# Kernel optimization log

Hardware: AMD Instinct MI355X
Metric: run time of the kernel (lower is better)

Reference implementation:

```python
import jax, jax.numpy as jnp
import numpy as np

D_MODEL = 1024
D_HEAD = 128


def setup_inputs() -> dict:
    key = jax.random.key(0)
    kx, kq, kk, kv, ko = jax.random.split(key, 5)
    x = jax.random.normal(kx, (4, 2048, D_MODEL), dtype=jnp.float32)
    # xavier-uniform-ish init scale
    s_in = (6.0 / (D_MODEL + D_HEAD)) ** 0.5
    wq = jax.random.uniform(kq, (D_MODEL, D_HEAD), minval=-s_in, maxval=s_in, dtype=jnp.float32)
    wk = jax.random.uniform(kk, (D_MODEL, D_HEAD), minval=-s_in, maxval=s_in, dtype=jnp.float32)
    wv = jax.random.uniform(kv, (D_MODEL, D_HEAD), minval=-s_in, maxval=s_in, dtype=jnp.float32)
    wo = jax.random.uniform(ko, (D_HEAD, D_MODEL), minval=-s_in, maxval=s_in, dtype=jnp.float32)
    return {"x": x, "wq": wq, "wk": wk, "wv": wv, "wo": wo}


def reference(x, wq, wk, wv, wo):
    # x: [b, s, d_model]
    s = x.shape[1]
    scale = 1.0 / (D_HEAD ** 0.5)
    q = jnp.einsum('bsd,dh->bsh', x, wq)
    k = jnp.einsum('bsd,dh->bsh', x, wk)
    v = jnp.einsum('bsd,dh->bsh', x, wv)
    scores = jnp.einsum('bqh,bkh->bqk', q, k) * scale  # [b, s, s]
    causal = jnp.tril(jnp.ones((s, s), dtype=bool))
    scores = jnp.where(causal, scores, -jnp.inf)
    attn = jax.nn.softmax(scores, axis=-1)
    ctx = jnp.einsum('bqk,bkh->bqh', attn, v)
    return jnp.einsum('bsh,hd->bsd', ctx, wo)
```

## Files before the change

kernel.cpp:

```cpp
#include <hip/hip_runtime.h>
#include <hip/hip_bf16.h>

typedef _Float16 half8 __attribute__((ext_vector_type(8)));
typedef _Float16 half4_t __attribute__((ext_vector_type(4)));
typedef _Float16 half2_t __attribute__((ext_vector_type(2)));
typedef float floatx4 __attribute__((ext_vector_type(4)));

#define MFMA16(a, b, c) __builtin_amdgcn_mfma_f32_16x16x32_f16(a, b, c, 0, 0, 0)
#define MASKVAL (-30000.0f)

#define QSCALE 0.1275261529f

__global__ __launch_bounds__(256) void transpose_convert(
    const float* __restrict__ wq, const float* __restrict__ wk,
    const float* __restrict__ wv, const float* __restrict__ wo,
    _Float16* __restrict__ wqt, _Float16* __restrict__ wkt,
    _Float16* __restrict__ wvt, _Float16* __restrict__ wot) {
  __shared__ float T[32][36];
  int bx = blockIdx.x, tid = threadIdx.x;
  const float* src;
  _Float16* dst;
  int R, C, r0, c0;
  if (bx < 384) {
    int p = bx >> 7, t = bx & 127;
    src = (p == 0) ? wq : (p == 1) ? wk : wv;
    dst = (p == 0) ? wqt : (p == 1) ? wkt : wvt;
    R = 1024; C = 128;
    r0 = (t & 31) * 32; c0 = (t >> 5) * 32;
  } else {
    int t = bx - 384;
    src = wo; dst = wot;
    R = 128; C = 1024;
    r0 = (t & 3) * 32; c0 = (t >> 2) * 32;
  }
  {
    int row = tid >> 3, c4 = (tid & 7) * 4;
    float4 f = *(const float4*)&src[(size_t)(r0 + row) * C + c0 + c4];
    T[row][c4] = f.x; T[row][c4 + 1] = f.y; T[row][c4 + 2] = f.z; T[row][c4 + 3] = f.w;
  }
  __syncthreads();
  {
    int cc = tid >> 3, r4 = (tid & 7) * 4;
    half4_t h;
    h[0] = (_Float16)T[r4 + 0][cc];
    h[1] = (_Float16)T[r4 + 1][cc];
    h[2] = (_Float16)T[r4 + 2][cc];
    h[3] = (_Float16)T[r4 + 3][cc];
    *(half4_t*)&dst[(size_t)(c0 + cc) * R + r0 + r4] = h;
  }
}

__global__ __launch_bounds__(256) void qkv_gemm(
    const float* __restrict__ x, const _Float16* __restrict__ wqt,
    const _Float16* __restrict__ wkt, const _Float16* __restrict__ wvt,
    _Float16* __restrict__ Qh, _Float16* __restrict__ Kh,
    _Float16* __restrict__ Vt) {
  __shared__ _Float16 A_lds[64 * 72];
  __shared__ _Float16 B_lds[128 * 72];
  int tid = threadIdx.x;
  int w = tid >> 6, lane = tid & 63, quad = lane >> 4, l16 = lane & 15;
  int m0 = blockIdx.x * 64;
  int proj = blockIdx.y;
  const _Float16* wt = (proj == 0) ? wqt : (proj == 1) ? wkt : wvt;
  floatx4 zero = {0.f, 0.f, 0.f, 0.f};
  floatx4 acc[8];
#pragma unroll
  for (int t = 0; t < 8; t++) acc[t] = zero;

  int arow = tid >> 2, akk = (tid & 3) * 16;
  int bn = tid >> 1, bkk = (tid & 1) * 32;

  for (int k0 = 0; k0 < 1024; k0 += 64) {
    {
      const float* s = x + (size_t)(m0 + arow) * 1024 + k0 + akk;
      float4 f0 = *(const float4*)(s);
      float4 f1 = *(const float4*)(s + 4);
      float4 f2 = *(const float4*)(s + 8);
      float4 f3 = *(const float4*)(s + 12);
      half8 h0, h1;
      h0[0] = (_Float16)f0.x; h0[1] = (_Float16)f0.y; h0[2] = (_Float16)f0.z; h0[3] = (_Float16)f0.w;
      h0[4] = (_Float16)f1.x; h0[5] = (_Float16)f1.y; h0[6] = (_Float16)f1.z; h0[7] = (_Float16)f1.w;
      h1[0] = (_Float16)f2.x; h1[1] = (_Float16)f2.y; h1[2] = (_Float16)f2.z; h1[3] = (_Float16)f2.w;
      h1[4] = (_Float16)f3.x; h1[5] = (_Float16)f3.y; h1[6] = (_Float16)f3.z; h1[7] = (_Float16)f3.w;
      *(half8*)&A_lds[arow * 72 + akk] = h0;
      *(half8*)&A_lds[arow * 72 + akk + 8] = h1;
    }
#pragma unroll
    for (int i = 0; i < 4; i++)
      *(half8*)&B_lds[bn * 72 + bkk + i * 8] =
          *(const half8*)&wt[(size_t)bn * 1024 + k0 + bkk + i * 8];
    __syncthreads();
    half8 a[2];
#pragma unroll
    for (int c = 0; c < 2; c++) a[c] = *(const half8*)&A_lds[(w * 16 + l16) * 72 + c * 32 + quad * 8];
#pragma unroll
    for (int t = 0; t < 8; t++)
#pragma unroll
      for (int c = 0; c < 2; c++) {
        half8 b = *(const half8*)&B_lds[(t * 16 + l16) * 72 + c * 32 + quad * 8];
        acc[t] = MFMA16(a[c], b, acc[t]);
      }
    __syncthreads();
  }
#pragma unroll
  for (int t = 0; t < 8; t++)
#pragma unroll
    for (int r = 0; r < 4; r++) {
      int row = m0 + w * 16 + quad * 4 + r;
      int col = t * 16 + l16;
      float v = acc[t][r];
      if (proj == 0)
        Qh[(size_t)row * 128 + col] = (_Float16)(v * QSCALE);
      else if (proj == 1)
        Kh[(size_t)row * 128 + col] = (_Float16)v;
      else {
        int bb = row >> 11, s = row & 2047;
        Vt[((size_t)(bb * 128 + col)) * 2048 + s] = (_Float16)v;
      }
    }
}

__global__ __launch_bounds__(256) void attn_partial(
    const _Float16* __restrict__ Qh, const _Float16* __restrict__ Kh,
    const _Float16* __restrict__ Vt, _Float16* __restrict__ Opart,
    float* __restrict__ Ml) {
  __shared__ _Float16 K_lds[64 * 136];
  __shared__ _Float16 V_lds[128 * 72];
  __shared__ _Float16 P_lds[4 * 16 * 76];
  int tid = threadIdx.x;
  int w = tid >> 6, lane = tid & 63, quad = lane >> 4, l16 = lane & 15;
  int kc = blockIdx.x;
  int qt = 31 - (int)blockIdx.y;
  int b = blockIdx.z;
  int q0 = qt * 64;
  int nkc = (q0 + 319) >> 8;
  if (kc >= nkc) return;
  int sidx = (b * 32 + qt) * 8 + kc;
  int ks0 = kc * 256;
  int kend = ks0 + 256 < q0 + 64 ? ks0 + 256 : q0 + 64;
  int qw0 = q0 + w * 16;

  const _Float16* Kb = Kh + (size_t)b * 2048 * 128;
  const _Float16* Vb = Vt + (size_t)b * 128 * 2048;

  half8 aq[4];
  {
    const _Float16* qbase = Qh + (size_t)(b * 2048 + qw0 + l16) * 128;
#pragma unroll
    for (int c = 0; c < 4; c++) aq[c] = *(const half8*)&qbase[c * 32 + quad * 8];
  }

  float m_r[4], l_r[4];
  floatx4 zero = {0.f, 0.f, 0.f, 0.f};
  floatx4 O[8];
#pragma unroll
  for (int r = 0; r < 4; r++) { m_r[r] = MASKVAL; l_r[r] = 0.f; }
#pragma unroll
  for (int t = 0; t < 8; t++) O[t] = zero;

  int krow = tid >> 2, kof = (tid & 3) * 32;
  int vh = tid & 127, vof = (tid >> 7) * 32;

  for (int ks = ks0; ks < kend; ks += 64) {
#pragma unroll
    for (int i = 0; i < 4; i++)
      *(half8*)&K_lds[krow * 136 + kof + i * 8] =
          *(const half8*)&Kb[(size_t)(ks + krow) * 128 + kof + i * 8];
#pragma unroll
    for (int i = 0; i < 4; i++)
      *(half8*)&V_lds[vh * 72 + vof + i * 8] =
          *(const half8*)&Vb[(size_t)vh * 2048 + ks + vof + i * 8];
    __syncthreads();

    if (ks <= qw0) {
      floatx4 sa[4];
#pragma unroll
      for (int t = 0; t < 4; t++) sa[t] = zero;
#pragma unroll
      for (int t = 0; t < 4; t++)
#pragma unroll
        for (int c = 0; c < 4; c++) {
          half8 bk = *(const half8*)&K_lds[(t * 16 + l16) * 136 + c * 32 + quad * 8];
          sa[t] = MFMA16(aq[c], bk, sa[t]);
        }

      bool domask = (ks + 63 > qw0);
      float p[4][4];
#pragma unroll
      for (int r = 0; r < 4; r++) {
        int query = qw0 + quad * 4 + r;
        float mx = m_r[r];
#pragma unroll
        for (int t = 0; t < 4; t++) {
          float s = sa[t][r];
          if (domask && (ks + t * 16 + l16 > query)) s = MASKVAL;
          p[t][r] = s;
          mx = fmaxf(mx, s);
        }
#pragma unroll
        for (int off = 1; off < 16; off <<= 1) mx = fmaxf(mx, __shfl_xor(mx, off));
        float alpha = exp2f(m_r[r] - mx);
        float rs = 0.f;
#pragma unroll
        for (int t = 0; t < 4; t++) {
          float e = exp2f(p[t][r] - mx);
          p[t][r] = e;
          rs += e;
        }
#pragma unroll
        for (int off = 1; off < 16; off <<= 1) rs += __shfl_xor(rs, off);
        l_r[r] = alpha * l_r[r] + rs;
        m_r[r] = mx;
#pragma unroll
        for (int t = 0; t < 8; t++) O[t][r] *= alpha;
      }

#pragma unroll
      for (int r = 0; r < 4; r++)
#pragma unroll
        for (int t = 0; t < 4; t++)
          P_lds[w * 16 * 76 + (quad * 4 + r) * 76 + t * 16 + l16] = (_Float16)p[t][r];

#pragma unroll
      for (int c2 = 0; c2 < 2; c2++) {
        half8 ap = *(const half8*)&P_lds[w * 16 * 76 + l16 * 76 + c2 * 32 + quad * 8];
#pragma unroll
        for (int t = 0; t < 8; t++) {
          half8 bv = *(const half8*)&V_lds[(t * 16 + l16) * 72 + c2 * 32 + quad * 8];
          O[t] = MFMA16(ap, bv, O[t]);
        }
      }
    }
    __syncthreads();
  }

  size_t obase = (size_t)sidx * 8192;
#pragma unroll
  for (int t = 0; t < 8; t++)
#pragma unroll
    for (int r = 0; r < 4; r++)
      Opart[obase + (size_t)(w * 16 + quad * 4 + r) * 128 + t * 16 + l16] = (_Float16)O[t][r];
  if (l16 == 0)
#pragma unroll
    for (int r = 0; r < 4; r++) {
      int row = w * 16 + quad * 4 + r;
      Ml[(size_t)sidx * 128 + row * 2] = m_r[r];
      Ml[(size_t)sidx * 128 + row * 2 + 1] = l_r[r];
    }
}

__global__ __launch_bounds__(256) void attn_combine(
    const _Float16* __restrict__ Opart, const float* __restrict__ Ml,
    _Float16* __restrict__ ctx) {
  int tid = threadIdx.x;
  int w = tid >> 6, lane = tid & 63;
  int row = blockIdx.x * 4 + w;
  int b = row >> 11, s = row & 2047;
  int qt = s >> 6, ri = s & 63;
  int nkc = (qt * 64 + 319) >> 8;
  int sidx0 = (b * 32 + qt) * 8;
  float m[8], l[8];
  float M = MASKVAL;
  for (int i = 0; i < nkc; i++) {
    m[i] = Ml[(size_t)(sidx0 + i) * 128 + ri * 2];
    l[i] = Ml[(size_t)(sidx0 + i) * 128 + ri * 2 + 1];
    M = fmaxf(M, m[i]);
  }
  float L = 0.f, sc[8];
  for (int i = 0; i < nkc; i++) {
    sc[i] = exp2f(m[i] - M);
    L += l[i] * sc[i];
  }
  float inv = 1.f / L;
  float a0 = 0.f, a1 = 0.f;
  for (int i = 0; i < nkc; i++) {
    half2_t o = *(const half2_t*)&Opart[(size_t)(sidx0 + i) * 8192 + (size_t)ri * 128 + lane * 2];
    a0 += sc[i] * (float)o[0];
    a1 += sc[i] * (float)o[1];
  }
  half2_t hv;
  hv[0] = (_Float16)(a0 * inv);
  hv[1] = (_Float16)(a1 * inv);
  *(half2_t*)&ctx[(size_t)row * 128 + lane * 2] = hv;
}

__global__ __launch_bounds__(256) void out_gemm(
    const _Float16* __restrict__ ctx, const _Float16* __restrict__ wot,
    float* __restrict__ out) {
  __shared__ _Float16 A_lds[64 * 136];
  __shared__ _Float16 B_lds[128 * 136];
  int tid = threadIdx.x;
  int w = tid >> 6, lane = tid & 63, quad = lane >> 4, l16 = lane & 15;
  int m0 = blockIdx.x * 64, n0 = blockIdx.y * 128;
  {
    int row = tid >> 2, kk = (tid & 3) * 32;
#pragma unroll
    for (int i = 0; i < 4; i++)
      *(half8*)&A_lds[row * 136 + kk + i * 8] =
          *(const half8*)&ctx[(size_t)(m0 + row) * 128 + kk + i * 8];
  }
  {
    int n = tid >> 1, kk = (tid & 1) * 64;
#pragma unroll
    for (int i = 0; i < 8; i++)
      *(half8*)&B_lds[n * 136 + kk + i * 8] =
          *(const half8*)&wot[(size_t)(n0 + n) * 128 + kk + i * 8];
  }
  __syncthreads();
  floatx4 zero = {0.f, 0.f, 0.f, 0.f};
  floatx4 acc[8];
#pragma unroll
  for (int t = 0; t < 8; t++) acc[t] = zero;
  half8 a[4];
#pragma unroll
  for (int c = 0; c < 4; c++) a[c] = *(const half8*)&A_lds[(w * 16 + l16) * 136 + c * 32 + quad * 8];
#pragma unroll
  for (int t = 0; t < 8; t++)
#pragma unroll
    for (int c = 0; c < 4; c++) {
      half8 b = *(const half8*)&B_lds[(t * 16 + l16) * 136 + c * 32 + quad * 8];
      acc[t] = MFMA16(a[c], b, acc[t]);
    }
#pragma unroll
  for (int t = 0; t < 8; t++)
#pragma unroll
    for (int r = 0; r < 4; r++) {
      int row = m0 + w * 16 + quad * 4 + r;
      out[(size_t)row * 1024 + n0 + t * 16 + l16] = acc[t][r];
    }
}

extern "C" void kernel_launch(void* const* d_in, const int* in_sizes, int n_in,
                              void* d_out, int out_size, void* d_ws, size_t ws_size,
                              hipStream_t stream) {
  const float* x = (const float*)d_in[0];
  const float* wq = (const float*)d_in[1];
  const float* wk = (const float*)d_in[2];
  const float* wv = (const float*)d_in[3];
  const float* wo = (const float*)d_in[4];
  char* ws = (char*)d_ws;
  _Float16* wqt = (_Float16*)(ws + 0);
  _Float16* wkt = (_Float16*)(ws + 262144);
  _Float16* wvt = (_Float16*)(ws + 524288);
  _Float16* wot = (_Float16*)(ws + 786432);
  _Float16* Qh  = (_Float16*)(ws + 1048576);
  _Float16* Kh  = (_Float16*)(ws + 1048576 + 2097152);
  _Float16* Vt  = (_Float16*)(ws + 1048576 + 2 * 2097152);
  _Float16* ctxh = (_Float16*)(ws + 1048576 + 3 * 2097152);
  _Float16* Opart = (_Float16*)(ws + 9437184);
  float* Ml = (float*)(ws + 9437184 + 16777216);
  float* out = (float*)d_out;

  transpose_convert<<<512, 256, 0, stream>>>(wq, wk, wv, wo, wqt, wkt, wvt, wot);
  qkv_gemm<<<dim3(128, 3), 256, 0, stream>>>(x, wqt, wkt, wvt, Qh, Kh, Vt);
  attn_partial<<<dim3(8, 32, 4), 256, 0, stream>>>(Qh, Kh, Vt, Opart, Ml);
  attn_combine<<<2048, 256, 0, stream>>>(Opart, Ml, ctxh);
  out_gemm<<<dim3(128, 8), 256, 0, stream>>>(ctxh, wot, out);
}
```

Baseline: 171.6 us.

## Pre-convert x to fp16, widen GEMM K-tile, split attention into single 128-key chunks

Adds a prep pass that converts x to fp16 and folds the Q scale into the transposed Wq weights, so the QKV GEMM loads fp16 directly with a 128-wide K tile. Attention partials now use one 128-key chunk per block (16 splits instead of 8), with no inner loop or online rescaling, and skip fully-masked tiles. Combine is simplified to a single pass. This raises parallelism and cuts per-block serial work, at the cost of an extra write and read of x in fp16 and more partial outputs for the combine step to read.

```diff
diff --git a/kernel.cpp b/kernel.cpp
--- a/kernel.cpp
+++ b/kernel.cpp
@@ -8,27 +8,40 @@
 
 #define MFMA16(a, b, c) __builtin_amdgcn_mfma_f32_16x16x32_f16(a, b, c, 0, 0, 0)
 #define MASKVAL (-30000.0f)
-
 #define QSCALE 0.1275261529f
 
-__global__ __launch_bounds__(256) void transpose_convert(
-    const float* __restrict__ wq, const float* __restrict__ wk,
-    const float* __restrict__ wv, const float* __restrict__ wo,
+__global__ __launch_bounds__(256) void prep(
+    const float* __restrict__ x, const float* __restrict__ wq,
+    const float* __restrict__ wk, const float* __restrict__ wv,
+    const float* __restrict__ wo, _Float16* __restrict__ xh,
     _Float16* __restrict__ wqt, _Float16* __restrict__ wkt,
     _Float16* __restrict__ wvt, _Float16* __restrict__ wot) {
+  int bx = blockIdx.x, tid = threadIdx.x;
+  if (bx < 4096) {
+    size_t idx = (size_t)bx * 2048 + tid * 8;
+    float4 f0 = *(const float4*)&x[idx];
+    float4 f1 = *(const float4*)&x[idx + 4];
+    half8 h;
+    h[0] = (_Float16)f0.x; h[1] = (_Float16)f0.y; h[2] = (_Float16)f0.z; h[3] = (_Float16)f0.w;
+    h[4] = (_Float16)f1.x; h[5] = (_Float16)f1.y; h[6] = (_Float16)f1.z; h[7] = (_Float16)f1.w;
+    *(half8*)&xh[idx] = h;
+    return;
+  }
   __shared__ float T[32][36];
-  int bx = blockIdx.x, tid = threadIdx.x;
   const float* src;
   _Float16* dst;
   int R, C, r0, c0;
-  if (bx < 384) {
-    int p = bx >> 7, t = bx & 127;
+  float sc = 1.0f;
+  if (bx < 4480) {
+    int b2 = bx - 4096;
+    int p = b2 >> 7, t = b2 & 127;
     src = (p == 0) ? wq : (p == 1) ? wk : wv;
     dst = (p == 0) ? wqt : (p == 1) ? wkt : wvt;
+    if (p == 0) sc = QSCALE;
     R = 1024; C = 128;
     r0 = (t & 31) * 32; c0 = (t >> 5) * 32;
   } else {
-    int t = bx - 384;
+    int t = bx - 4480;
     src = wo; dst = wot;
     R = 128; C = 1024;
     r0 = (t & 3) * 32; c0 = (t >> 2) * 32;
@@ -42,21 +55,21 @@
   {
     int cc = tid >> 3, r4 = (tid & 7) * 4;
     half4_t h;
-    h[0] = (_Float16)T[r4 + 0][cc];
-    h[1] = (_Float16)T[r4 + 1][cc];
-    h[2] = (_Float16)T[r4 + 2][cc];
-    h[3] = (_Float16)T[r4 + 3][cc];
+    h[0] = (_Float16)(T[r4 + 0][cc] * sc);
+    h[1] = (_Float16)(T[r4 + 1][cc] * sc);
+    h[2] = (_Float16)(T[r4 + 2][cc] * sc);
+    h[3] = (_Float16)(T[r4 + 3][cc] * sc);
     *(half4_t*)&dst[(size_t)(c0 + cc) * R + r0 + r4] = h;
   }
 }
 
 __global__ __launch_bounds__(256) void qkv_gemm(
-    const float* __restrict__ x, const _Float16* __restrict__ wqt,
+    const _Float16* __restrict__ xh, const _Float16* __restrict__ wqt,
     const _Float16* __restrict__ wkt, const _Float16* __restrict__ wvt,
     _Float16* __restrict__ Qh, _Float16* __restrict__ Kh,
     _Float16* __restrict__ Vt) {
-  __shared__ _Float16 A_lds[64 * 72];
-  __shared__ _Float16 B_lds[128 * 72];
+  __shared__ _Float16 A_lds[64 * 136];
+  __shared__ _Float16 B_lds[128 * 136];
   int tid = threadIdx.x;
   int w = tid >> 6, lane = tid & 63, quad = lane >> 4, l16 = lane & 15;
   int m0 = blockIdx.x * 64;
@@ -67,37 +80,28 @@
 #pragma unroll
   for (int t = 0; t < 8; t++) acc[t] = zero;
 
-  int arow = tid >> 2, akk = (tid & 3) * 16;
-  int bn = tid >> 1, bkk = (tid & 1) * 32;
-
-  for (int k0 = 0; k0 < 1024; k0 += 64) {
-    {
-      const float* s = x + (size_t)(m0 + arow) * 1024 + k0 + akk;
-      float4 f0 = *(const float4*)(s);
-      float4 f1 = *(const float4*)(s + 4);
-      float4 f2 = *(const float4*)(s + 8);
-      float4 f3 = *(const float4*)(s + 12);
-      half8 h0, h1;
-      h0[0] = (_Float16)f0.x; h0[1] = (_Float16)f0.y; h0[2] = (_Float16)f0.z; h0[3] = (_Float16)f0.w;
-      h0[4] = (_Float16)f1.x; h0[5] = (_Float16)f1.y; h0[6] = (_Float16)f1.z; h0[7] = (_Float16)f1.w;
-      h1[0] = (_Float16)f2.x; h1[1] = (_Float16)f2.y; h1[2] = (_Float16)f2.z; h1[3] = (_Float16)f2.w;
-      h1[4] = (_Float16)f3.x; h1[5] = (_Float16)f3.y; h1[6] = (_Float16)f3.z; h1[7] = (_Float16)f3.w;
-      *(half8*)&A_lds[arow * 72 + akk] = h0;
-      *(half8*)&A_lds[arow * 72 + akk + 8] = h1;
-    }
+  int arow = tid >> 2, akk = (tid & 3) * 32;
+  int brow = tid >> 1, bkk = (tid & 1) * 64;
+
+  for (int k0 = 0; k0 < 1024; k0 += 128) {
 #pragma unroll
     for (int i = 0; i < 4; i++)
-      *(half8*)&B_lds[bn * 72 + bkk + i * 8] =
-          *(const half8*)&wt[(size_t)bn * 1024 + k0 + bkk + i * 8];
+      *(half8*)&A_lds[arow * 136 + akk + i * 8] =
+          *(const half8*)&xh[(size_t)(m0 + arow) * 1024 + k0 + akk + i * 8];
+#pragma unroll
+    for (int i = 0; i < 8; i++)
+      *(half8*)&B_lds[brow * 136 + bkk + i * 8] =
+          *(const half8*)&wt[(size_t)brow * 1024 + k0 + bkk + i * 8];
     __syncthreads();
-    half8 a[2];
-#pragma unroll
-    for (int c = 0; c < 2; c++) a[c] = *(const half8*)&A_lds[(w * 16 + l16) * 72 + c * 32 + quad * 8];
+    half8 a[4];
+#pragma unroll
+    for (int c = 0; c < 4; c++)
+      a[c] = *(const half8*)&A_lds[(w * 16 + l16) * 136 + c * 32 + quad * 8];
 #pragma unroll
     for (int t = 0; t < 8; t++)
 #pragma unroll
-      for (int c = 0; c < 2; c++) {
-        half8 b = *(const half8*)&B_lds[(t * 16 + l16) * 72 + c * 32 + quad * 8];
+      for (int c = 0; c < 4; c++) {
+        half8 b = *(const half8*)&B_lds[(t * 16 + l16) * 136 + c * 32 + quad * 8];
         acc[t] = MFMA16(a[c], b, acc[t]);
       }
     __syncthreads();
@@ -108,14 +112,14 @@
     for (int r = 0; r < 4; r++) {
       int row = m0 + w * 16 + quad * 4 + r;
       int col = t * 16 + l16;
-      float v = acc[t][r];
+      _Float16 v = (_Float16)acc[t][r];
       if (proj == 0)
-        Qh[(size_t)row * 128 + col] = (_Float16)(v * QSCALE);
+        Qh[(size_t)row * 128 + col] = v;
       else if (proj == 1)
-        Kh[(size_t)row * 128 + col] = (_Float16)v;
+        Kh[(size_t)row * 128 + col] = v;
       else {
         int bb = row >> 11, s = row & 2047;
-        Vt[((size_t)(bb * 128 + col)) * 2048 + s] = (_Float16)v;
+        Vt[((size_t)(bb * 128 + col)) * 2048 + s] = v;
       }
     }
 }
@@ -124,115 +128,116 @@
     const _Float16* __restrict__ Qh, const _Float16* __restrict__ Kh,
     const _Float16* __restrict__ Vt, _Float16* __restrict__ Opart,
     float* __restrict__ Ml) {
-  __shared__ _Float16 K_lds[64 * 136];
-  __shared__ _Float16 V_lds[128 * 72];
-  __shared__ _Float16 P_lds[4 * 16 * 76];
+  __shared__ _Float16 K_lds[128 * 136];
+  __shared__ _Float16 V_lds[128 * 136];
   int tid = threadIdx.x;
   int w = tid >> 6, lane = tid & 63, quad = lane >> 4, l16 = lane & 15;
   int kc = blockIdx.x;
   int qt = 31 - (int)blockIdx.y;
   int b = blockIdx.z;
+  int nkc = (qt + 2) >> 1;
+  if (kc >= nkc) return;
   int q0 = qt * 64;
-  int nkc = (q0 + 319) >> 8;
-  if (kc >= nkc) return;
-  int sidx = (b * 32 + qt) * 8 + kc;
-  int ks0 = kc * 256;
-  int kend = ks0 + 256 < q0 + 64 ? ks0 + 256 : q0 + 64;
+  int k0 = kc * 128;
   int qw0 = q0 + w * 16;
+  int sidx = (b * 32 + qt) * 16 + kc;
+  bool domask = (kc == nkc - 1);
 
   const _Float16* Kb = Kh + (size_t)b * 2048 * 128;
   const _Float16* Vb = Vt + (size_t)b * 128 * 2048;
 
+  {
+    int row = tid >> 1, koff = (tid & 1) * 64;
+#pragma unroll
+    for (int i = 0; i < 8; i++)
+      *(half8*)&K_lds[row * 136 + koff + i * 8] =
+          *(const half8*)&Kb[(size_t)(k0 + row) * 128 + koff + i * 8];
+#pragma unroll
+    for (int i = 0; i < 8; i++)
+      *(half8*)&V_lds[row * 136 + koff + i * 8] =
+          *(const half8*)&Vb[(size_t)row * 2048 + k0 + koff + i * 8];
+  }
+
   half8 aq[4];
   {
     const _Float16* qbase = Qh + (size_t)(b * 2048 + qw0 + l16) * 128;
 #pragma unroll
     for (int c = 0; c < 4; c++) aq[c] = *(const half8*)&qbase[c * 32 + quad * 8];
   }
+  __syncthreads();
+
+  int ntl = ((qw0 + 15 - k0) >> 4) + 1;
+  ntl = ntl > 8 ? 8 : ntl;
+
+  floatx4 zero = {0.f, 0.f, 0.f, 0.f};
+  floatx4 sa[8];
+#pragma unroll
+  for (int t = 0; t < 8; t++) sa[t] = zero;
+#pragma unroll
+  for (int t = 0; t < 8; t++)
+    if (t < ntl) {
+#pragma unroll
+      for (int c = 0; c < 4; c++) {
+        half8 bk = *(const half8*)&K_lds[(t * 16 + l16) * 136 + c * 32 + quad * 8];
+        sa[t] = MFMA16(aq[c], bk, sa[t]);
+      }
+    }
 
   float m_r[4], l_r[4];
-  floatx4 zero = {0.f, 0.f, 0.f, 0.f};
+  float p[8][4];
+#pragma unroll
+  for (int r = 0; r < 4; r++) {
+    int query = qw0 + quad * 4 + r;
+    float mx = MASKVAL;
+#pragma unroll
+    for (int t = 0; t < 8; t++) {
+      if (t < ntl) {
+        float s = sa[t][r];
+        if (domask && (k0 + t * 16 + l16 > query)) s = MASKVAL;
+        p[t][r] = s;
+        mx = fmaxf(mx, s);
+      } else {
+        p[t][r] = 0.f;
+      }
+    }
+#pragma unroll
+    for (int off = 1; off < 16; off <<= 1) mx = fmaxf(mx, __shfl_xor(mx, off));
+    float rs = 0.f;
+#pragma unroll
+    for (int t = 0; t < 8; t++)
+      if (t < ntl) {
+        float e = exp2f(p[t][r] - mx);
+        p[t][r] = e;
+        rs += e;
+      }
+#pragma unroll
+    for (int off = 1; off < 16; off <<= 1) rs += __shfl_xor(rs, off);
+    m_r[r] = mx;
+    l_r[r] = rs;
+  }
+
+  __syncthreads();
+  _Float16* P = K_lds + w * 16 * 136;
+#pragma unroll
+  for (int r = 0; r < 4; r++)
+#pragma unroll
+    for (int t = 0; t < 8; t++)
+      P[(quad * 4 + r) * 136 + t * 16 + l16] = (_Float16)p[t][r];
+
   floatx4 O[8];
 #pragma unroll
-  for (int r = 0; r < 4; r++) { m_r[r] = MASKVAL; l_r[r] = 0.f; }
-#pragma unroll
   for (int t = 0; t < 8; t++) O[t] = zero;
-
-  int krow = tid >> 2, kof = (tid & 3) * 32;
-  int vh = tid & 127, vof = (tid >> 7) * 32;
-
-  for (int ks = ks0; ks < kend; ks += 64) {
-#pragma unroll
-    for (int i = 0; i < 4; i++)
-      *(half8*)&K_lds[krow * 136 + kof + i * 8] =
-          *(const half8*)&Kb[(size_t)(ks + krow) * 128 + kof + i * 8];
-#pragma unroll
-    for (int i = 0; i < 4; i++)
-      *(half8*)&V_lds[vh * 72 + vof + i * 8] =
-          *(const half8*)&Vb[(size_t)vh * 2048 + ks + vof + i * 8];
-    __syncthreads();
-
-    if (ks <= qw0) {
-      floatx4 sa[4];
-#pragma unroll
-      for (int t = 0; t < 4; t++) sa[t] = zero;
-#pragma unroll
-      for (int t = 0; t < 4; t++)
-#pragma unroll
-        for (int c = 0; c < 4; c++) {
-          half8 bk = *(const half8*)&K_lds[(t * 16 + l16) * 136 + c * 32 + quad * 8];
-          sa[t] = MFMA16(aq[c], bk, sa[t]);
-        }
-
-      bool domask = (ks + 63 > qw0);
-      float p[4][4];
-#pragma unroll
-      for (int r = 0; r < 4; r++) {
-        int query = qw0 + quad * 4 + r;
-        float mx = m_r[r];
-#pragma unroll
-        for (int t = 0; t < 4; t++) {
-          float s = sa[t][r];
-          if (domask && (ks + t * 16 + l16 > query)) s = MASKVAL;
-          p[t][r] = s;
-          mx = fmaxf(mx, s);
-        }
-#pragma unroll
-        for (int off = 1; off < 16; off <<= 1) mx = fmaxf(mx, __shfl_xor(mx, off));
-        float alpha = exp2f(m_r[r] - mx);
-        float rs = 0.f;
-#pragma unroll
-        for (int t = 0; t < 4; t++) {
-          float e = exp2f(p[t][r] - mx);
-          p[t][r] = e;
-          rs += e;
-        }
-#pragma unroll
-        for (int off = 1; off < 16; off <<= 1) rs += __shfl_xor(rs, off);
-        l_r[r] = alpha * l_r[r] + rs;
-        m_r[r] = mx;
-#pragma unroll
-        for (int t = 0; t < 8; t++) O[t][r] *= alpha;
-      }
-
-#pragma unroll
-      for (int r = 0; r < 4; r++)
-#pragma unroll
-        for (int t = 0; t < 4; t++)
-          P_lds[w * 16 * 76 + (quad * 4 + r) * 76 + t * 16 + l16] = (_Float16)p[t][r];
-
-#pragma unroll
-      for (int c2 = 0; c2 < 2; c2++) {
-        half8 ap = *(const half8*)&P_lds[w * 16 * 76 + l16 * 76 + c2 * 32 + quad * 8];
-#pragma unroll
-        for (int t = 0; t < 8; t++) {
-          half8 bv = *(const half8*)&V_lds[(t * 16 + l16) * 72 + c2 * 32 + quad * 8];
-          O[t] = MFMA16(ap, bv, O[t]);
-        }
-      }
-    }
-    __syncthreads();
-  }
+  int nc2 = (ntl + 1) >> 1;
+#pragma unroll
+  for (int c2 = 0; c2 < 4; c2++)
+    if (c2 < nc2) {
+      half8 ap = *(const half8*)&P[l16 * 136 + c2 * 32 + quad * 8];
+#pragma unroll
+      for (int t = 0; t < 8; t++) {
+        half8 bv = *(const half8*)&V_lds[(t * 16 + l16) * 136 + c2 * 32 + quad * 8];
+        O[t] = MFMA16(ap, bv, O[t]);
+      }
+    }
 
   size_t obase = (size_t)sidx * 8192;
 #pragma unroll
@@ -257,27 +262,22 @@
   int row = blockIdx.x * 4 + w;
   int b = row >> 11, s = row & 2047;
   int qt = s >> 6, ri = s & 63;
-  int nkc = (qt * 64 + 319) >> 8;
-  int sidx0 = (b * 32 + qt) * 8;
-  float m[8], l[8];
+  int nkc = (qt + 2) >> 1;
+  int sidx0 = (b * 32 + qt) * 16;
   float M = MASKVAL;
+  for (int i = 0; i < nkc; i++)
+    M = fmaxf(M, Ml[(size_t)(sidx0 + i) * 128 + ri * 2]);
+  float L = 0.f, a0 = 0.f, a1 = 0.f;
   for (int i = 0; i < nkc; i++) {
-    m[i] = Ml[(size_t)(sidx0 + i) * 128 + ri * 2];
-    l[i] = Ml[(size_t)(sidx0 + i) * 128 + ri * 2 + 1];
-    M = fmaxf(M, m[i]);
-  }
-  float L = 0.f, sc[8];
-  for (int i = 0; i < nkc; i++) {
-    sc[i] = exp2f(m[i] - M);
-    L += l[i] * sc[i];
+    float mi = Ml[(size_t)(sidx0 + i) * 128 + ri * 2];
+    float li = Ml[(size_t)(sidx0 + i) * 128 + ri * 2 + 1];
+    float sc = exp2f(mi - M);
+    L += li * sc;
+    half2_t o = *(const half2_t*)&Opart[(size_t)(sidx0 + i) * 8192 + (size_t)ri * 128 + lane * 2];
+    a0 += sc * (float)o[0];
+    a1 += sc * (float)o[1];
   }
   float inv = 1.f / L;
-  float a0 = 0.f, a1 = 0.f;
-  for (int i = 0; i < nkc; i++) {
-    half2_t o = *(const half2_t*)&Opart[(size_t)(sidx0 + i) * 8192 + (size_t)ri * 128 + lane * 2];
-    a0 += sc[i] * (float)o[0];
-    a1 += sc[i] * (float)o[1];
-  }
   half2_t hv;
   hv[0] = (_Float16)(a0 * inv);
   hv[1] = (_Float16)(a1 * inv);
@@ -343,17 +343,18 @@
   _Float16* wkt = (_Float16*)(ws + 262144);
   _Float16* wvt = (_Float16*)(ws + 524288);
   _Float16* wot = (_Float16*)(ws + 786432);
-  _Float16* Qh  = (_Float16*)(ws + 1048576);
-  _Float16* Kh  = (_Float16*)(ws + 1048576 + 2097152);
-  _Float16* Vt  = (_Float16*)(ws + 1048576 + 2 * 2097152);
-  _Float16* ctxh = (_Float16*)(ws + 1048576 + 3 * 2097152);
-  _Float16* Opart = (_Float16*)(ws + 9437184);
-  float* Ml = (float*)(ws + 9437184 + 16777216);
+  _Float16* xh  = (_Float16*)(ws + 1048576);
+  _Float16* Qh  = (_Float16*)(ws + 17825792);
+  _Float16* Kh  = (_Float16*)(ws + 19922944);
+  _Float16* Vt  = (_Float16*)(ws + 22020096);
+  _Float16* ctxh = (_Float16*)(ws + 24117248);
+  _Float16* Opart = (_Float16*)(ws + 26214400);
+  float* Ml = (float*)(ws + 59768832);
   float* out = (float*)d_out;
 
-  transpose_convert<<<512, 256, 0, stream>>>(wq, wk, wv, wo, wqt, wkt, wvt, wot);
-  qkv_gemm<<<dim3(128, 3), 256, 0, stream>>>(x, wqt, wkt, wvt, Qh, Kh, Vt);
-  attn_partial<<<dim3(8, 32, 4), 256, 0, stream>>>(Qh, Kh, Vt, Opart, Ml);
+  prep<<<4608, 256, 0, stream>>>(x, wq, wk, wv, wo, xh, wqt, wkt, wvt, wot);
+  qkv_gemm<<<dim3(128, 3), 256, 0, stream>>>(xh, wqt, wkt, wvt, Qh, Kh, Vt);
+  attn_partial<<<dim3(16, 32, 4), 256, 0, stream>>>(Qh, Kh, Vt, Opart, Ml);
   attn_combine<<<2048, 256, 0, stream>>>(Opart, Ml, ctxh);
   out_gemm<<<dim3(128, 8), 256, 0, stream>>>(ctxh, wot, out);
 }
```

Result: no change. 172.7 us (+0.6%).
